# Kernel tuning notes

Hardware: AMD Instinct MI355X
Metric: run time of the kernel (lower is better)

The kernel has to match this reference:

```python
import jax, jax.numpy as jnp
import numpy as np

B, L, E, H = 2, 2048, 512, 8
D = E // H  # head_dim = 64


def setup_inputs() -> dict:
    key = jax.random.key(0)
    ks = jax.random.split(key, 12)
    s = 0.02
    return {
        "values": jax.random.normal(ks[0], (B, L, E), jnp.float32),
        "keys": jax.random.normal(ks[1], (B, L, E), jnp.float32),
        "query": jax.random.normal(ks[2], (B, L, E), jnp.float32),
        "mask": jax.random.randint(ks[3], (B, 1, L, L), 0, 2, jnp.int32),
        "Wv": jax.random.normal(ks[4], (E, E), jnp.float32) * s,
        "bv": jax.random.normal(ks[5], (E,), jnp.float32) * s,
        "Wk": jax.random.normal(ks[6], (E, E), jnp.float32) * s,
        "bk": jax.random.normal(ks[7], (E,), jnp.float32) * s,
        "Wq": jax.random.normal(ks[8], (E, E), jnp.float32) * s,
        "bq": jax.random.normal(ks[9], (E,), jnp.float32) * s,
        "Wo": jax.random.normal(ks[10], (E, E), jnp.float32) * s,
        "bo": jax.random.normal(ks[11], (E,), jnp.float32) * s,
    }


def reference(values, keys, query, mask, Wv, bv, Wk, bk, Wq, bq, Wo, bo):
    b, lq = query.shape[0], query.shape[1]
    # torch Linear: y = x @ W.T + b
    v = (values @ Wv.T + bv).reshape(b, -1, H, D)
    k = (keys @ Wk.T + bk).reshape(b, -1, H, D)
    q = (query @ Wq.T + bq).reshape(b, lq, H, D)
    energy = jnp.einsum("bqhd,bkhd->bhqk", q, k)  # [B,H,Lq,Lk]
    # mask applied BEFORE the scale, as in the original
    energy = jnp.where(mask == 0, jnp.float32(-1e20), energy)
    # NOTE: scales by sqrt(embed_size), not sqrt(head_dim) (faithful)
    attn = jax.nn.softmax(energy / jnp.sqrt(jnp.float32(E)), axis=3)
    out = jnp.einsum("bhql,blhd->bqhd", attn, v).reshape(b, lq, E)
    return out @ Wo.T + bo
```

## Files before the change

### kernel.cpp

```cpp
#include <hip/hip_runtime.h>
#include <hip/hip_bf16.h>
#include <math.h>

#define BB 2
#define LL 2048
#define EE 512
#define HH 8
#define DD 64
#define MM (BB * LL)
#define LW (LL / 64)

typedef short bf16x8 __attribute__((ext_vector_type(8)));
typedef float f32x4 __attribute__((ext_vector_type(4)));

#define MFMA16(a, b, c) __builtin_amdgcn_mfma_f32_16x16x32_bf16((a), (b), (c), 0, 0, 0)

#if __has_builtin(__builtin_amdgcn_exp2f)
#define EXP2(x) __builtin_amdgcn_exp2f(x)
#else
#define EXP2(x) exp2f(x)
#endif

#define QSCALE 0.0637587146f

__device__ __forceinline__ void gl2lds16(const __hip_bfloat16* g, __hip_bfloat16* l) {
    __builtin_amdgcn_global_load_lds(
        (const __attribute__((address_space(1))) unsigned int*)(g),
        (__attribute__((address_space(3))) unsigned int*)(l),
        16, 0, 0);
}

__device__ __forceinline__ uint4 cvt8_bf16(const float4 a, const float4 b) {
    union { __hip_bfloat16 h[8]; uint4 u; } t;
    t.h[0] = __float2bfloat16(a.x); t.h[1] = __float2bfloat16(a.y);
    t.h[2] = __float2bfloat16(a.z); t.h[3] = __float2bfloat16(a.w);
    t.h[4] = __float2bfloat16(b.x); t.h[5] = __float2bfloat16(b.y);
    t.h[6] = __float2bfloat16(b.z); t.h[7] = __float2bfloat16(b.w);
    return t.u;
}

struct PrepArgs {
    const float* xsrc[3];
    __hip_bfloat16* xdst[3];
    const float* wsrc[4];
    __hip_bfloat16* wdst[4];
    const int* mask;
    unsigned long long* mbits;
};

__global__ __launch_bounds__(256) void prep(PrepArgs a) {
    const int blk = blockIdx.x;
    if (blk < 3072) {
        const int t = blk >> 10;
        const int i = ((blk & 1023) * 256 + threadIdx.x) * 8;
        const float* s = a.xsrc[t] + i;
        float4 f0 = *(const float4*)(s);
        float4 f1 = *(const float4*)(s + 4);
        *(uint4*)(a.xdst[t] + i) = cvt8_bf16(f0, f1);
    } else if (blk < 3584) {
        const int r = blk - 3072;
        const int t = r >> 7;
        const int i = ((r & 127) * 256 + threadIdx.x) * 8;
        const float* s = a.wsrc[t] + i;
        float4 f0 = *(const float4*)(s);
        float4 f1 = *(const float4*)(s + 4);
        *(uint4*)(a.wdst[t] + i) = cvt8_bf16(f0, f1);
    } else {
        const int mb = blk - 3584;
        #pragma unroll
        for (int r = 0; r < 16; ++r) {
            const size_t idx = ((size_t)mb * 16 + r) * 256 + threadIdx.x;
            const int m = a.mask[idx];
            const unsigned long long w = __ballot(m != 0);
            if ((threadIdx.x & 63) == 0) a.mbits[idx >> 6] = w;
        }
    }
}

__global__ __launch_bounds__(256) void transpose_v(
    const __hip_bfloat16* __restrict__ vb, __hip_bfloat16* __restrict__ vt) {
    __shared__ __hip_bfloat16 T[64][72];
    const int tid = threadIdx.x;
    const int l0 = blockIdx.x * 64;
    const int h = blockIdx.y;
    const int b = blockIdx.z;
    const int row = tid >> 2;
    const int cg = (tid & 3) * 16;

    const __hip_bfloat16* src = vb + ((size_t)b * LL + l0 + row) * EE + h * DD + cg;
    *(uint4*)&T[row][cg] = *(const uint4*)src;
    *(uint4*)&T[row][cg + 8] = *(const uint4*)(src + 8);
    __syncthreads();

    __hip_bfloat16 t[16];
    #pragma unroll
    for (int e = 0; e < 16; ++e) t[e] = T[cg + e][row];
    __hip_bfloat16* dst = vt + (((size_t)b * HH + h) * DD + row) * LL + l0 + cg;
    *(uint4*)&dst[0] = *(uint4*)&t[0];
    *(uint4*)&dst[8] = *(uint4*)&t[8];
}

struct QKVArgs {
    const __hip_bfloat16* X[3];
    const __hip_bfloat16* W[3];
    const float* bias[3];
    __hip_bfloat16* O[3];
};

__global__ __launch_bounds__(256) void gemm_qkv(QKVArgs p) {
    __shared__ __hip_bfloat16 As[2][2][64][32];
    __shared__ __hip_bfloat16 Bs[2][2][128][32];

    const int z = blockIdx.z;
    const __hip_bfloat16* __restrict__ X = p.X[z];
    const __hip_bfloat16* __restrict__ W = p.W[z];
    const float* __restrict__ bias = p.bias[z];
    __hip_bfloat16* __restrict__ O = p.O[z];
    const float oscale = (z == 0) ? QSCALE : 1.0f;

    const int tid = threadIdx.x;
    const int wave = tid >> 6, lane = tid & 63;
    const int l15 = lane & 15, quad = lane >> 4;
    const int wn = wave * 32;
    const int m0 = blockIdx.y * 64, n0 = blockIdx.x * 128;

    const int lr = lane >> 2;
    const int lc = (lane & 3) * 8;
    const __hip_bfloat16* Ax = X + (size_t)(m0 + wave * 16 + lr) * EE + lc;
    const __hip_bfloat16* Bx = W + (size_t)(n0 + wave * 32 + lr) * EE + lc;

    f32x4 acc[4][2] = {};

    #define STAGE_G(buf, k0)                                                   \
        gl2lds16(Ax + (k0),           &As[buf][0][wave * 16][0]);              \
        gl2lds16(Ax + (k0) + 32,      &As[buf][1][wave * 16][0]);              \
        gl2lds16(Bx + (k0),           &Bs[buf][0][wave * 32][0]);              \
        gl2lds16(Bx + (k0) + 32,      &Bs[buf][1][wave * 32][0]);              \
        gl2lds16(Bx + (k0) + 16 * EE,      &Bs[buf][0][wave * 32 + 16][0]);    \
        gl2lds16(Bx + (k0) + 16 * EE + 32, &Bs[buf][1][wave * 32 + 16][0]);

    STAGE_G(0, 0);
    __syncthreads();

    for (int kt = 0; kt < 8; ++kt) {
        const int cur = kt & 1;
        if (kt < 7) { STAGE_G(cur ^ 1, (kt + 1) * 64); }

        #pragma unroll
        for (int c = 0; c < 2; ++c) {
            bf16x8 af[4], bf2[2];
            #pragma unroll
            for (int i = 0; i < 4; ++i)
                af[i] = *(const bf16x8*)&As[cur][c][i * 16 + l15][quad * 8];
            #pragma unroll
            for (int j = 0; j < 2; ++j)
                bf2[j] = *(const bf16x8*)&Bs[cur][c][wn + j * 16 + l15][quad * 8];
            #pragma unroll
            for (int i = 0; i < 4; ++i)
                #pragma unroll
                for (int j = 0; j < 2; ++j)
                    acc[i][j] = MFMA16(af[i], bf2[j], acc[i][j]);
        }
        __syncthreads();
    }

    #pragma unroll
    for (int i = 0; i < 4; ++i)
        #pragma unroll
        for (int j = 0; j < 2; ++j) {
            const int n = n0 + wn + j * 16 + l15;
            const float bv = bias[n];
            #pragma unroll
            for (int reg = 0; reg < 4; ++reg) {
                const int m = m0 + i * 16 + quad * 4 + reg;
                O[(size_t)m * EE + n] = __float2bfloat16((acc[i][j][reg] + bv) * oscale);
            }
        }
}

__global__ __launch_bounds__(256) void gemm_out(
    const __hip_bfloat16* __restrict__ X, const __hip_bfloat16* __restrict__ W,
    const float* __restrict__ bias, float* __restrict__ C) {
    __shared__ __hip_bfloat16 As[2][2][64][32];
    __shared__ __hip_bfloat16 Bs[2][2][128][32];

    const int tid = threadIdx.x;
    const int wave = tid >> 6, lane = tid & 63;
    const int l15 = lane & 15, quad = lane >> 4;
    const int wn = wave * 32;
    const int m0 = blockIdx.y * 64, n0 = blockIdx.x * 128;

    const int lr = lane >> 2;
    const int lc = (lane & 3) * 8;
    const __hip_bfloat16* Ax = X + (size_t)(m0 + wave * 16 + lr) * EE + lc;
    const __hip_bfloat16* Bx = W + (size_t)(n0 + wave * 32 + lr) * EE + lc;

    f32x4 acc[4][2] = {};

    STAGE_G(0, 0);
    __syncthreads();

    for (int kt = 0; kt < 8; ++kt) {
        const int cur = kt & 1;
        if (kt < 7) { STAGE_G(cur ^ 1, (kt + 1) * 64); }

        #pragma unroll
        for (int c = 0; c < 2; ++c) {
            bf16x8 af[4], bf2[2];
            #pragma unroll
            for (int i = 0; i < 4; ++i)
                af[i] = *(const bf16x8*)&As[cur][c][i * 16 + l15][quad * 8];
            #pragma unroll
            for (int j = 0; j < 2; ++j)
                bf2[j] = *(const bf16x8*)&Bs[cur][c][wn + j * 16 + l15][quad * 8];
            #pragma unroll
            for (int i = 0; i < 4; ++i)
                #pragma unroll
                for (int j = 0; j < 2; ++j)
                    acc[i][j] = MFMA16(af[i], bf2[j], acc[i][j]);
        }
        __syncthreads();
    }

    #pragma unroll
    for (int i = 0; i < 4; ++i)
        #pragma unroll
        for (int j = 0; j < 2; ++j) {
            const int n = n0 + wn + j * 16 + l15;
            const float bv = bias[n];
            #pragma unroll
            for (int reg = 0; reg < 4; ++reg) {
                const int m = m0 + i * 16 + quad * 4 + reg;
                C[(size_t)m * EE + n] = acc[i][j][reg] + bv;
            }
        }
}

__global__ __launch_bounds__(256) void attn_mfma(
    const __hip_bfloat16* __restrict__ Qb, const __hip_bfloat16* __restrict__ Kb,
    const __hip_bfloat16* __restrict__ vtg, const unsigned long long* __restrict__ mbits,
    __hip_bfloat16* __restrict__ Op) {
    __shared__ __hip_bfloat16 Ks[2][2][64][32];
    __shared__ __hip_bfloat16 Vs[2][2][64][32];
    __shared__ __hip_bfloat16 Ps[4][16][72];

    const int tid = threadIdx.x;
    const int wave = tid >> 6;
    const int lane = tid & 63;
    const int l15 = lane & 15;
    const int quad = lane >> 4;
    const int b = blockIdx.z;
    const int h = blockIdx.y;
    const int q0 = blockIdx.x * 64;
    const int myq = q0 + wave * 16 + l15;

    bf16x8 qf[2];
    {
        const __hip_bfloat16* qrow = Qb + ((size_t)b * LL + myq) * EE + h * DD;
        qf[0] = *(const bf16x8*)(qrow + quad * 8);
        qf[1] = *(const bf16x8*)(qrow + 32 + quad * 8);
    }

    const int lr = lane >> 2;
    const int lc = (lane & 3) * 8;
    const __hip_bfloat16* Kx = Kb + ((size_t)b * LL + wave * 16 + lr) * EE + h * DD + lc;
    const __hip_bfloat16* Vx = vtg + (((size_t)b * HH + h) * DD + wave * 16 + lr) * LL + lc;
    const unsigned long long* mrow = mbits + ((size_t)b * LL + myq) * LW;

    f32x4 o[4] = {};
    float lr0 = 0.f, lr1 = 0.f;

    #define STAGE_KV(buf, k0)                                                  \
        gl2lds16(Kx + (size_t)(k0) * EE,      &Ks[buf][0][wave * 16][0]);      \
        gl2lds16(Kx + (size_t)(k0) * EE + 32, &Ks[buf][1][wave * 16][0]);      \
        gl2lds16(Vx + (k0),                   &Vs[buf][0][wave * 16][0]);      \
        gl2lds16(Vx + (k0) + 32,              &Vs[buf][1][wave * 16][0]);

    STAGE_KV(0, 0);
    unsigned long long mw_cur = mrow[0];
    __syncthreads();

    for (int t = 0; t < LW; ++t) {
        const int cur = t & 1;
        unsigned long long mw_n;
        if (t + 1 < LW) {
            STAGE_KV(cur ^ 1, (t + 1) * 64);
            mw_n = mrow[t + 1];
        }

        f32x4 st[4] = {};
        #pragma unroll
        for (int mt = 0; mt < 4; ++mt) {
            bf16x8 a0 = *(const bf16x8*)&Ks[cur][0][mt * 16 + l15][quad * 8];
            bf16x8 a1 = *(const bf16x8*)&Ks[cur][1][mt * 16 + l15][quad * 8];
            st[mt] = MFMA16(a0, qf[0], st[mt]);
            st[mt] = MFMA16(a1, qf[1], st[mt]);
        }

        #pragma unroll
        for (int mt = 0; mt < 4; ++mt) {
            float p[4];
            #pragma unroll
            for (int reg = 0; reg < 4; ++reg) {
                const bool live = (mw_cur >> (mt * 16 + quad * 4 + reg)) & 1ull;
                const float e = EXP2(st[mt][reg]);
                p[reg] = live ? e : 0.f;
            }
            lr0 += p[0] + p[1];
            lr1 += p[2] + p[3];
            union { __hip_bfloat16 hh[4]; ushort4 v; } pk;
            pk.hh[0] = __float2bfloat16(p[0]);
            pk.hh[1] = __float2bfloat16(p[1]);
            pk.hh[2] = __float2bfloat16(p[2]);
            pk.hh[3] = __float2bfloat16(p[3]);
            *(ushort4*)&Ps[wave][l15][mt * 16 + quad * 4] = pk.v;
        }

        bf16x8 pa0 = *(const bf16x8*)&Ps[wave][l15][quad * 8];
        bf16x8 pa1 = *(const bf16x8*)&Ps[wave][l15][32 + quad * 8];
        #pragma unroll
        for (int nt = 0; nt < 4; ++nt) {
            bf16x8 vb0 = *(const bf16x8*)&Vs[cur][0][nt * 16 + l15][quad * 8];
            bf16x8 vb1 = *(const bf16x8*)&Vs[cur][1][nt * 16 + l15][quad * 8];
            o[nt] = MFMA16(pa0, vb0, o[nt]);
            o[nt] = MFMA16(pa1, vb1, o[nt]);
        }

        if (t + 1 < LW) mw_cur = mw_n;
        __syncthreads();
    }

    float lrun = lr0 + lr1;
    lrun += __shfl_xor(lrun, 16);
    lrun += __shfl_xor(lrun, 32);
    const float linv = 1.f / lrun;
    float linvR[4];
    #pragma unroll
    for (int reg = 0; reg < 4; ++reg)
        linvR[reg] = __shfl(linv, quad * 4 + reg);

    __hip_bfloat16* Ob = Op + ((size_t)b * LL + q0 + wave * 16) * EE + h * DD;
    #pragma unroll
    for (int nt = 0; nt < 4; ++nt)
        #pragma unroll
        for (int reg = 0; reg < 4; ++reg) {
            const int qrow = quad * 4 + reg;
            Ob[(size_t)qrow * EE + nt * 16 + l15] =
                __float2bfloat16(o[nt][reg] * linvR[reg]);
        }
}

extern "C" void kernel_launch(void* const* d_in, const int* in_sizes, int n_in,
                              void* d_out, int out_size, void* d_ws, size_t ws_size,
                              hipStream_t stream) {
    const float* values = (const float*)d_in[0];
    const float* keys   = (const float*)d_in[1];
    const float* query  = (const float*)d_in[2];
    const int*   mask   = (const int*)d_in[3];
    const float* Wv = (const float*)d_in[4];
    const float* bv = (const float*)d_in[5];
    const float* Wk = (const float*)d_in[6];
    const float* bk = (const float*)d_in[7];
    const float* Wq = (const float*)d_in[8];
    const float* bq = (const float*)d_in[9];
    const float* Wo = (const float*)d_in[10];
    const float* bo = (const float*)d_in[11];
    float* out = (float*)d_out;

    const size_t XS = (size_t)MM * EE * 2;
    const size_t WS = (size_t)EE * EE * 2;
    char* w = (char*)d_ws;
    __hip_bfloat16* xq  = (__hip_bfloat16*)(w);
    __hip_bfloat16* xk  = (__hip_bfloat16*)(w + XS);
    __hip_bfloat16* xv  = (__hip_bfloat16*)(w + 2 * XS);
    __hip_bfloat16* qb  = (__hip_bfloat16*)(w + 3 * XS);
    __hip_bfloat16* kb  = (__hip_bfloat16*)(w + 4 * XS);
    __hip_bfloat16* vb  = (__hip_bfloat16*)(w + 5 * XS);
    __hip_bfloat16* vtg = (__hip_bfloat16*)(w + 6 * XS);
    __hip_bfloat16* aob = (__hip_bfloat16*)(w + 7 * XS);
    __hip_bfloat16* wqb = (__hip_bfloat16*)(w + 8 * XS);
    __hip_bfloat16* wkb = (__hip_bfloat16*)(w + 8 * XS + WS);
    __hip_bfloat16* wvb = (__hip_bfloat16*)(w + 8 * XS + 2 * WS);
    __hip_bfloat16* wob = (__hip_bfloat16*)(w + 8 * XS + 3 * WS);
    unsigned long long* mbits = (unsigned long long*)(w + 8 * XS + 4 * WS);

    PrepArgs pa;
    pa.xsrc[0] = query; pa.xsrc[1] = keys; pa.xsrc[2] = values;
    pa.xdst[0] = xq;    pa.xdst[1] = xk;   pa.xdst[2] = xv;
    pa.wsrc[0] = Wq; pa.wsrc[1] = Wk; pa.wsrc[2] = Wv; pa.wsrc[3] = Wo;
    pa.wdst[0] = wqb; pa.wdst[1] = wkb; pa.wdst[2] = wvb; pa.wdst[3] = wob;
    pa.mask = mask; pa.mbits = mbits;

    QKVArgs qa;
    qa.X[0] = xq;  qa.X[1] = xk;  qa.X[2] = xv;
    qa.W[0] = wqb; qa.W[1] = wkb; qa.W[2] = wvb;
    qa.bias[0] = bq; qa.bias[1] = bk; qa.bias[2] = bv;
    qa.O[0] = qb;  qa.O[1] = kb;  qa.O[2] = vb;

    prep<<<5632, 256, 0, stream>>>(pa);
    gemm_qkv<<<dim3(EE / 128, MM / 64, 3), 256, 0, stream>>>(qa);
    transpose_v<<<dim3(LL / 64, HH, BB), 256, 0, stream>>>(vb, vtg);
    attn_mfma<<<dim3(LL / 64, HH, BB), 256, 0, stream>>>(qb, kb, vtg, mbits, aob);
    gemm_out<<<dim3(EE / 128, MM / 64), 256, 0, stream>>>(aob, wob, bo, out);
}
```

Measured before the change: 190.4 us.

## Fuse V transpose into QKV GEMM epilogue and register-stage K/V in attention

The V projection epilogue now writes its output directly in the [B,H,D,L] transposed layout, so the separate transpose_v kernel and its intermediate buffer are removed. The attention kernel swaps its async global-to-LDS copies for register-staged loads into padded unsplit LDS tiles, with the stores issued after the PV MFMAs. It also packs P into bf16 pairs and keeps a single row-sum accumulator. The transposed epilogue writes are strided 8-byte stores that may coalesce poorly, and register staging raises register pressure in exchange for hiding load latency behind compute.

```diff
diff --git a/kernel.cpp b/kernel.cpp
--- a/kernel.cpp
+++ b/kernel.cpp
@@ -77,29 +77,6 @@
     }
 }
 
-__global__ __launch_bounds__(256) void transpose_v(
-    const __hip_bfloat16* __restrict__ vb, __hip_bfloat16* __restrict__ vt) {
-    __shared__ __hip_bfloat16 T[64][72];
-    const int tid = threadIdx.x;
-    const int l0 = blockIdx.x * 64;
-    const int h = blockIdx.y;
-    const int b = blockIdx.z;
-    const int row = tid >> 2;
-    const int cg = (tid & 3) * 16;
-
-    const __hip_bfloat16* src = vb + ((size_t)b * LL + l0 + row) * EE + h * DD + cg;
-    *(uint4*)&T[row][cg] = *(const uint4*)src;
-    *(uint4*)&T[row][cg + 8] = *(const uint4*)(src + 8);
-    __syncthreads();
-
-    __hip_bfloat16 t[16];
-    #pragma unroll
-    for (int e = 0; e < 16; ++e) t[e] = T[cg + e][row];
-    __hip_bfloat16* dst = vt + (((size_t)b * HH + h) * DD + row) * LL + l0 + cg;
-    *(uint4*)&dst[0] = *(uint4*)&t[0];
-    *(uint4*)&dst[8] = *(uint4*)&t[8];
-}
-
 struct QKVArgs {
     const __hip_bfloat16* X[3];
     const __hip_bfloat16* W[3];
@@ -116,7 +93,6 @@
     const __hip_bfloat16* __restrict__ W = p.W[z];
     const float* __restrict__ bias = p.bias[z];
     __hip_bfloat16* __restrict__ O = p.O[z];
-    const float oscale = (z == 0) ? QSCALE : 1.0f;
 
     const int tid = threadIdx.x;
     const int wave = tid >> 6, lane = tid & 63;
@@ -164,18 +140,37 @@
         __syncthreads();
     }
 
-    #pragma unroll
-    for (int i = 0; i < 4; ++i)
-        #pragma unroll
-        for (int j = 0; j < 2; ++j) {
-            const int n = n0 + wn + j * 16 + l15;
-            const float bv = bias[n];
-            #pragma unroll
-            for (int reg = 0; reg < 4; ++reg) {
-                const int m = m0 + i * 16 + quad * 4 + reg;
-                O[(size_t)m * EE + n] = __float2bfloat16((acc[i][j][reg] + bv) * oscale);
+    if (z == 2) {
+        #pragma unroll
+        for (int i = 0; i < 4; ++i)
+            #pragma unroll
+            for (int j = 0; j < 2; ++j) {
+                const int n = n0 + wn + j * 16 + l15;
+                const float bv = bias[n];
+                const int h = n >> 6, d = n & 63;
+                union { __hip_bfloat16 hh[4]; ushort4 v4; } pk;
+                #pragma unroll
+                for (int reg = 0; reg < 4; ++reg)
+                    pk.hh[reg] = __float2bfloat16(acc[i][j][reg] + bv);
+                const int m = m0 + i * 16 + quad * 4;
+                const int bb = m >> 11, l = m & 2047;
+                *(ushort4*)&O[(((size_t)bb * HH + h) * DD + d) * LL + l] = pk.v4;
             }
-        }
+    } else {
+        const float oscale = (z == 0) ? QSCALE : 1.0f;
+        #pragma unroll
+        for (int i = 0; i < 4; ++i)
+            #pragma unroll
+            for (int j = 0; j < 2; ++j) {
+                const int n = n0 + wn + j * 16 + l15;
+                const float bv = bias[n];
+                #pragma unroll
+                for (int reg = 0; reg < 4; ++reg) {
+                    const int m = m0 + i * 16 + quad * 4 + reg;
+                    O[(size_t)m * EE + n] = __float2bfloat16((acc[i][j][reg] + bv) * oscale);
+                }
+            }
+    }
 }
 
 __global__ __launch_bounds__(256) void gemm_out(
@@ -240,9 +235,9 @@
     const __hip_bfloat16* __restrict__ Qb, const __hip_bfloat16* __restrict__ Kb,
     const __hip_bfloat16* __restrict__ vtg, const unsigned long long* __restrict__ mbits,
     __hip_bfloat16* __restrict__ Op) {
-    __shared__ __hip_bfloat16 Ks[2][2][64][32];
-    __shared__ __hip_bfloat16 Vs[2][2][64][32];
-    __shared__ __hip_bfloat16 Ps[4][16][72];
+    __shared__ __hip_bfloat16 Ks[2][64][68];
+    __shared__ __hip_bfloat16 Vs[2][64][68];
+    __shared__ __hip_bfloat16 Ps[4][16][68];
 
     const int tid = threadIdx.x;
     const int wave = tid >> 6;
@@ -254,6 +249,9 @@
     const int q0 = blockIdx.x * 64;
     const int myq = q0 + wave * 16 + l15;
 
+    const int srow = tid >> 2;
+    const int scg = (tid & 3) * 16;
+
     bf16x8 qf[2];
     {
         const __hip_bfloat16* qrow = Qb + ((size_t)b * LL + myq) * EE + h * DD;
@@ -261,38 +259,48 @@
         qf[1] = *(const bf16x8*)(qrow + 32 + quad * 8);
     }
 
-    const int lr = lane >> 2;
-    const int lc = (lane & 3) * 8;
-    const __hip_bfloat16* Kx = Kb + ((size_t)b * LL + wave * 16 + lr) * EE + h * DD + lc;
-    const __hip_bfloat16* Vx = vtg + (((size_t)b * HH + h) * DD + wave * 16 + lr) * LL + lc;
+    const __hip_bfloat16* kbase = Kb + ((size_t)b * LL + srow) * EE + h * DD + scg;
+    const __hip_bfloat16* vbase = vtg + (((size_t)b * HH + h) * DD + srow) * LL + scg;
     const unsigned long long* mrow = mbits + ((size_t)b * LL + myq) * LW;
 
     f32x4 o[4] = {};
-    float lr0 = 0.f, lr1 = 0.f;
-
-    #define STAGE_KV(buf, k0)                                                  \
-        gl2lds16(Kx + (size_t)(k0) * EE,      &Ks[buf][0][wave * 16][0]);      \
-        gl2lds16(Kx + (size_t)(k0) * EE + 32, &Ks[buf][1][wave * 16][0]);      \
-        gl2lds16(Vx + (k0),                   &Vs[buf][0][wave * 16][0]);      \
-        gl2lds16(Vx + (k0) + 32,              &Vs[buf][1][wave * 16][0]);
-
-    STAGE_KV(0, 0);
+    float lrun = 0.f;
+
+    {
+        uint4 k0a = *(const uint4*)(kbase);
+        uint4 k0b = *(const uint4*)(kbase + 8);
+        uint4 v0a = *(const uint4*)(vbase);
+        uint4 v0b = *(const uint4*)(vbase + 8);
+        *(uint4*)&Ks[0][srow][scg] = k0a;
+        *(uint4*)&Ks[0][srow][scg + 8] = k0b;
+        *(uint4*)&Vs[0][srow][scg] = v0a;
+        *(uint4*)&Vs[0][srow][scg + 8] = v0b;
+    }
     unsigned long long mw_cur = mrow[0];
     __syncthreads();
 
     for (int t = 0; t < LW; ++t) {
         const int cur = t & 1;
+        const int nxt = cur ^ 1;
+        const bool more = (t + 1) < LW;
+
+        uint4 ka0, ka1, va0, va1;
         unsigned long long mw_n;
-        if (t + 1 < LW) {
-            STAGE_KV(cur ^ 1, (t + 1) * 64);
+        if (more) {
+            const __hip_bfloat16* kn = kbase + (size_t)(t + 1) * 64 * EE;
+            const __hip_bfloat16* vn = vbase + (t + 1) * 64;
+            ka0 = *(const uint4*)(kn);
+            ka1 = *(const uint4*)(kn + 8);
+            va0 = *(const uint4*)(vn);
+            va1 = *(const uint4*)(vn + 8);
             mw_n = mrow[t + 1];
         }
 
         f32x4 st[4] = {};
         #pragma unroll
         for (int mt = 0; mt < 4; ++mt) {
-            bf16x8 a0 = *(const bf16x8*)&Ks[cur][0][mt * 16 + l15][quad * 8];
-            bf16x8 a1 = *(const bf16x8*)&Ks[cur][1][mt * 16 + l15][quad * 8];
+            bf16x8 a0 = *(const bf16x8*)&Ks[cur][mt * 16 + l15][quad * 8];
+            bf16x8 a1 = *(const bf16x8*)&Ks[cur][mt * 16 + l15][32 + quad * 8];
             st[mt] = MFMA16(a0, qf[0], st[mt]);
             st[mt] = MFMA16(a1, qf[1], st[mt]);
         }
@@ -305,14 +313,11 @@
                 const bool live = (mw_cur >> (mt * 16 + quad * 4 + reg)) & 1ull;
                 const float e = EXP2(st[mt][reg]);
                 p[reg] = live ? e : 0.f;
+                lrun += p[reg];
             }
-            lr0 += p[0] + p[1];
-            lr1 += p[2] + p[3];
-            union { __hip_bfloat16 hh[4]; ushort4 v; } pk;
-            pk.hh[0] = __float2bfloat16(p[0]);
-            pk.hh[1] = __float2bfloat16(p[1]);
-            pk.hh[2] = __float2bfloat16(p[2]);
-            pk.hh[3] = __float2bfloat16(p[3]);
+            union { __hip_bfloat162 h2[2]; ushort4 v; } pk;
+            pk.h2[0] = __float22bfloat162_rn(make_float2(p[0], p[1]));
+            pk.h2[1] = __float22bfloat162_rn(make_float2(p[2], p[3]));
             *(ushort4*)&Ps[wave][l15][mt * 16 + quad * 4] = pk.v;
         }
 
@@ -320,17 +325,22 @@
         bf16x8 pa1 = *(const bf16x8*)&Ps[wave][l15][32 + quad * 8];
         #pragma unroll
         for (int nt = 0; nt < 4; ++nt) {
-            bf16x8 vb0 = *(const bf16x8*)&Vs[cur][0][nt * 16 + l15][quad * 8];
-            bf16x8 vb1 = *(const bf16x8*)&Vs[cur][1][nt * 16 + l15][quad * 8];
+            bf16x8 vb0 = *(const bf16x8*)&Vs[cur][nt * 16 + l15][quad * 8];
+            bf16x8 vb1 = *(const bf16x8*)&Vs[cur][nt * 16 + l15][32 + quad * 8];
             o[nt] = MFMA16(pa0, vb0, o[nt]);
             o[nt] = MFMA16(pa1, vb1, o[nt]);
         }
 
-        if (t + 1 < LW) mw_cur = mw_n;
+        if (more) {
+            *(uint4*)&Ks[nxt][srow][scg] = ka0;
+            *(uint4*)&Ks[nxt][srow][scg + 8] = ka1;
+            *(uint4*)&Vs[nxt][srow][scg] = va0;
+            *(uint4*)&Vs[nxt][srow][scg + 8] = va1;
+            mw_cur = mw_n;
+        }
         __syncthreads();
     }
 
-    float lrun = lr0 + lr1;
     lrun += __shfl_xor(lrun, 16);
     lrun += __shfl_xor(lrun, 32);
     const float linv = 1.f / lrun;
@@ -375,14 +385,13 @@
     __hip_bfloat16* xv  = (__hip_bfloat16*)(w + 2 * XS);
     __hip_bfloat16* qb  = (__hip_bfloat16*)(w + 3 * XS);
     __hip_bfloat16* kb  = (__hip_bfloat16*)(w + 4 * XS);
-    __hip_bfloat16* vb  = (__hip_bfloat16*)(w + 5 * XS);
-    __hip_bfloat16* vtg = (__hip_bfloat16*)(w + 6 * XS);
-    __hip_bfloat16* aob = (__hip_bfloat16*)(w + 7 * XS);
-    __hip_bfloat16* wqb = (__hip_bfloat16*)(w + 8 * XS);
-    __hip_bfloat16* wkb = (__hip_bfloat16*)(w + 8 * XS + WS);
-    __hip_bfloat16* wvb = (__hip_bfloat16*)(w + 8 * XS + 2 * WS);
-    __hip_bfloat16* wob = (__hip_bfloat16*)(w + 8 * XS + 3 * WS);
-    unsigned long long* mbits = (unsigned long long*)(w + 8 * XS + 4 * WS);
+    __hip_bfloat16* vtg = (__hip_bfloat16*)(w + 5 * XS);
+    __hip_bfloat16* aob = (__hip_bfloat16*)(w + 6 * XS);
+    __hip_bfloat16* wqb = (__hip_bfloat16*)(w + 7 * XS);
+    __hip_bfloat16* wkb = (__hip_bfloat16*)(w + 7 * XS + WS);
+    __hip_bfloat16* wvb = (__hip_bfloat16*)(w + 7 * XS + 2 * WS);
+    __hip_bfloat16* wob = (__hip_bfloat16*)(w + 7 * XS + 3 * WS);
+    unsigned long long* mbits = (unsigned long long*)(w + 7 * XS + 4 * WS);
 
     PrepArgs pa;
     pa.xsrc[0] = query; pa.xsrc[1] = keys; pa.xsrc[2] = values;
@@ -395,11 +404,10 @@
     qa.X[0] = xq;  qa.X[1] = xk;  qa.X[2] = xv;
     qa.W[0] = wqb; qa.W[1] = wkb; qa.W[2] = wvb;
     qa.bias[0] = bq; qa.bias[1] = bk; qa.bias[2] = bv;
-    qa.O[0] = qb;  qa.O[1] = kb;  qa.O[2] = vb;
+    qa.O[0] = qb;  qa.O[1] = kb;  qa.O[2] = vtg;
 
     prep<<<5632, 256, 0, stream>>>(pa);
     gemm_qkv<<<dim3(EE / 128, MM / 64, 3), 256, 0, stream>>>(qa);
-    transpose_v<<<dim3(LL / 64, HH, BB), 256, 0, stream>>>(vb, vtg);
     attn_mfma<<<dim3(LL / 64, HH, BB), 256, 0, stream>>>(qb, kb, vtg, mbits, aob);
     gemm_out<<<dim3(EE / 128, MM / 64), 256, 0, stream>>>(aob, wob, bo, out);
 }
```

New measurement: 186.3 us. 2.2% less time.
